# Kernel optimization log

Measured on AMD Instinct MI355X. Metric: run time of the kernel, lower is better.

Reference implementation:

```python
import jax, jax.numpy as jnp
import numpy as np

N = 50000
EPS = 1e-5


def _layernorm(x, g, b):
    mu = jnp.mean(x, axis=-1, keepdims=True)
    var = jnp.mean((x - mu) ** 2, axis=-1, keepdims=True)
    return (x - mu) * jax.lax.rsqrt(var + EPS) * g + b


def _gcn_conv(x, W, b, src, dst, norm, n):
    # PyG GCNConv: x' = D^{-1/2}(A+I)D^{-1/2} (x W) + b, self-loops already in src/dst
    xw = x @ W                                   # [N, F_out]
    msg = xw[src] * norm[:, None]                # gather + scale, [E+N, F_out]
    return jax.ops.segment_sum(msg, dst, num_segments=n) + b


def _prep_edges(edge_index, n):
    loops = jnp.arange(n, dtype=edge_index.dtype)
    src = jnp.concatenate([edge_index[0], loops])
    dst = jnp.concatenate([edge_index[1], loops])
    deg = jax.ops.segment_sum(jnp.ones(dst.shape[0], jnp.float32), dst, num_segments=n)
    dinv = jnp.where(deg > 0, jax.lax.rsqrt(deg), 0.0)
    norm = dinv[src] * dinv[dst]
    return src, dst, norm


def setup_inputs() -> dict:
    key = jax.random.key(0)
    ks = jax.random.split(key, 8)
    gene, hid, nc = 512, 256, 4
    x = jax.random.normal(ks[0], (N, gene), jnp.float32)
    edge_index = jax.random.randint(ks[1], (2, 1600000), 0, N, dtype=jnp.int64)

    def lin(k, fi, fo):
        return jax.random.normal(k, (fi, fo), jnp.float32) / np.sqrt(fi)

    d = {
        "x": x, "edge_index": edge_index,
        "W1": lin(ks[2], gene, hid), "b1": jnp.zeros(hid, jnp.float32),
        "W2": lin(ks[3], hid, 2 * hid), "b2": jnp.zeros(2 * hid, jnp.float32),
        "W3": lin(ks[4], 2 * hid, hid), "b3": jnp.zeros(hid, jnp.float32),
        "W4": lin(ks[5], hid, hid // 2), "b4": jnp.zeros(hid // 2, jnp.float32),
        "Wc": lin(ks[6], hid // 2, nc), "bc": jnp.zeros(nc, jnp.float32),
        "g1": jnp.ones(hid, jnp.float32), "be1": jnp.zeros(hid, jnp.float32),
        "g2": jnp.ones(2 * hid, jnp.float32), "be2": jnp.zeros(2 * hid, jnp.float32),
        "g3": jnp.ones(hid, jnp.float32), "be3": jnp.zeros(hid, jnp.float32),
        "g4": jnp.ones(hid // 2, jnp.float32), "be4": jnp.zeros(hid // 2, jnp.float32),
    }
    return d


def reference(x, edge_index, W1, b1, W2, b2, W3, b3, W4, b4, Wc, bc,
              g1, be1, g2, be2, g3, be3, g4, be4):
    n = x.shape[0]
    src, dst, norm = _prep_edges(edge_index, n)
    # dropout layers are identity (training=False)
    h1 = jax.nn.elu(_layernorm(_gcn_conv(x, W1, b1, src, dst, norm, n), g1, be1))
    h2 = jax.nn.elu(_layernorm(_gcn_conv(h1, W2, b2, src, dst, norm, n), g2, be2))
    h3 = jax.nn.elu(_layernorm(_gcn_conv(h2, W3, b3, src, dst, norm, n), g3, be3))
    h4_in = h3 + h1
    out_conv = _gcn_conv(h4_in, W4, b4, src, dst, norm, n)
    out_bn = _layernorm(out_conv, g4, be4)
    h = jax.nn.elu(out_bn)
    return (h @ Wc + bc, out_conv, out_bn)
```

## Files before the change

### kernel.cpp

```cpp
#include <hip/hip_runtime.h>
#include <hip/hip_bf16.h>
#include <math.h>

typedef unsigned short u16;
typedef u16 us8 __attribute__((ext_vector_type(8)));
typedef u16 us4 __attribute__((ext_vector_type(4)));
typedef float f32x4 __attribute__((ext_vector_type(4)));
typedef float f32x8 __attribute__((ext_vector_type(8)));
typedef __bf16 bf8 __attribute__((ext_vector_type(8)));

#define SCAN_B 256
#define CH 8192

__device__ __forceinline__ float bf2f(u16 v) {
    unsigned u = ((unsigned)v) << 16;
    return __builtin_bit_cast(float, u);
}
__device__ __forceinline__ u16 f2bf(float f) {
    unsigned u = __builtin_bit_cast(unsigned, f);
    unsigned lsb = (u >> 16) & 1;
    u += 0x7fff + lsb;
    return (u16)(u >> 16);
}
__device__ __forceinline__ void fma8(f32x8& acc, float w, us8 v) {
#pragma unroll
    for (int j = 0; j < 8; j++) acc[j] += w * bf2f(v[j]);
}

__global__ void detect_k(const int* __restrict__ ei, int E,
                         const u16* __restrict__ xraw, int* flag) {
    __shared__ int c_i32, c_f32;
    if (threadIdx.x == 0) { c_i32 = 0; c_f32 = 0; }
    __syncthreads();
    int ne = (E < 4096) ? E : 4096;
    for (int e = threadIdx.x; e < ne; e += blockDim.x)
        if (ei[2 * e + 1] != 0) c_i32 = 1;
    for (int k = threadIdx.x; k < 8192; k += blockDim.x) {
        u16 v = xraw[2 * k];
        int ex = (v >> 7) & 0xFF;
        if (ex >= 0xF0) atomicAdd(&c_f32, 1);
    }
    __syncthreads();
    if (threadIdx.x == 0) {
        flag[0] = (c_i32 == 0) ? 1 : 0;
        flag[1] = (c_f32 >= 4) ? 1 : 0;
    }
}

struct WEnt { const void* s; u16* dst; int K; int Nn; int base; };
struct PEnt { const void* s; int n; int off; };
struct PTab { PEnt e[14]; };

#define GX_CVT 4096

__global__ void megacvt_k(const void* __restrict__ xsrc, u16* __restrict__ xdst,
                          long nq, WEnt e0, WEnt e1, WEnt e2, WEnt e3, int wtotal,
                          PTab tab, float* __restrict__ pbuf,
                          const int* __restrict__ flag, int gw) {
    int f32m = flag[1];
    int bid = blockIdx.x;
    if (bid < GX_CVT) {
        long i0 = (long)bid * blockDim.x + threadIdx.x;
        long stride = (long)GX_CVT * blockDim.x;
        if (f32m) {
            const f32x4* s = (const f32x4*)xsrc;
            for (long i = i0; i < nq; i += stride) {
                f32x4 v = s[i];
                us4 o;
                #pragma unroll
                for (int j = 0; j < 4; j++) o[j] = f2bf(v[j]);
                ((us4*)xdst)[i] = o;
            }
        } else {
            const us4* s = (const us4*)xsrc;
            for (long i = i0; i < nq; i += stride) ((us4*)xdst)[i] = s[i];
        }
    } else if (bid < GX_CVT + gw) {
        int t = (bid - GX_CVT) * blockDim.x + threadIdx.x;
        if (t >= wtotal) return;
        WEnt en = (t >= e3.base) ? e3 : ((t >= e2.base) ? e2 : ((t >= e1.base) ? e1 : e0));
        int li = t - en.base;
        int k = li / en.Nn, nn = li - k * en.Nn;
        u16 b;
        if (f32m) b = f2bf(((const float*)en.s)[li]);
        else      b = ((const u16*)en.s)[li];
        en.dst[nn * en.K + k] = b;
    } else {
        PEnt en = tab.e[bid - GX_CVT - gw];
        for (int i = threadIdx.x; i < en.n; i += blockDim.x) {
            float v = f32m ? ((const float*)en.s)[i] : bf2f(((const u16*)en.s)[i]);
            pbuf[en.off + i] = v;
        }
    }
}

__global__ void histA_k(const int* __restrict__ ei, const int* __restrict__ flag,
                        int* __restrict__ hist, int* __restrict__ counts,
                        int E, int n, int NB, int NBUK, int shiftv) {
    __shared__ int lh[256];
    int blk = blockIdx.x;
    int gi = blk * 256 + threadIdx.x;
    if (gi < n) counts[gi] = 1;
    for (int b = threadIdx.x; b < NBUK; b += 256) lh[b] = 0;
    __syncthreads();
    int e0 = blk * CH;
    int e1 = min(e0 + CH, E);
    int i64 = flag[0];
    for (int e = e0 + threadIdx.x; e < e1; e += 256) {
        int d;
        if (i64) d = (int)((const long long*)ei)[(size_t)E + e];
        else     d = ei[(size_t)E + e];
        int b = ((unsigned)d < (unsigned)n) ? min(d >> shiftv, NBUK - 1) : (NBUK - 1);
        atomicAdd(&lh[b], 1);
    }
    __syncthreads();
    for (int b = threadIdx.x; b < NBUK; b += 256) hist[b * NB + blk] = lh[b];
}

__global__ void scan1_k(const int* __restrict__ counts, int* incl, int* bsum, int n) {
    __shared__ int tmp[SCAN_B];
    int t = threadIdx.x;
    int i = blockIdx.x * SCAN_B + t;
    int v = (i < n) ? counts[i] : 0;
    tmp[t] = v;
    __syncthreads();
    for (int o = 1; o < SCAN_B; o <<= 1) {
        int x = 0;
        if (t >= o) x = tmp[t - o];
        __syncthreads();
        if (t >= o) tmp[t] += x;
        __syncthreads();
    }
    if (i < n) incl[i] = tmp[t];
    if (t == SCAN_B - 1) bsum[blockIdx.x] = tmp[t];
}

__global__ void scan2_k(const int* __restrict__ bsum, int* bscan, int nb) {
    __shared__ int tmp[SCAN_B];
    int t = threadIdx.x;
    tmp[t] = (t < nb) ? bsum[t] : 0;
    __syncthreads();
    for (int o = 1; o < SCAN_B; o <<= 1) {
        int x = 0;
        if (t >= o) x = tmp[t - o];
        __syncthreads();
        if (t >= o) tmp[t] += x;
        __syncthreads();
    }
    bscan[t] = tmp[t];
}

__global__ void scatC_k(const int* __restrict__ ei, const int* __restrict__ flag,
                        const int* __restrict__ histincl, const int* __restrict__ bscan,
                        const int* __restrict__ hist, long long* __restrict__ ebuf,
                        int* __restrict__ counts,
                        int E, int n, int NB, int NBUK, int shiftv) {
    __shared__ int cur[256];
    int blk = blockIdx.x;
    for (int b = threadIdx.x; b < NBUK; b += 256) {
        int fi = b * NB + blk;
        int boff = (fi >= 256) ? bscan[(fi >> 8) - 1] : 0;
        cur[b] = histincl[fi] + boff - hist[fi];
    }
    __syncthreads();
    int e0 = blk * CH;
    int e1 = min(e0 + CH, E);
    int i64 = flag[0];
    for (int e = e0 + threadIdx.x; e < e1; e += 256) {
        int s, d;
        if (i64) {
            const long long* e64 = (const long long*)ei;
            s = (int)e64[e]; d = (int)e64[(size_t)E + e];
        } else {
            s = ei[e]; d = ei[(size_t)E + e];
        }
        int b = ((unsigned)d < (unsigned)n) ? min(d >> shiftv, NBUK - 1) : (NBUK - 1);
        int pos = atomicAdd(&cur[b], 1);
        ebuf[pos] = ((long long)(unsigned)d << 32) | (unsigned)s;
        if ((unsigned)d < (unsigned)n) atomicAdd(&counts[d], 1);
    }
}

__global__ void finCSR_k(const int* __restrict__ incl, const int* __restrict__ bscan,
                         const int* __restrict__ counts, int* __restrict__ rowptr,
                         int* __restrict__ cursor, float* __restrict__ dinv, int n) {
    int i = blockIdx.x * SCAN_B + threadIdx.x;
    if (i < n) {
        int boff = (blockIdx.x > 0) ? bscan[blockIdx.x - 1] : 0;
        int rp_end = incl[i] + boff;
        rowptr[i + 1] = rp_end;
        if (i == 0) rowptr[0] = 0;
        cursor[i] = rp_end - counts[i];
        dinv[i] = rsqrtf((float)counts[i]);
    }
}

__global__ void scatD_k(const long long* __restrict__ ebuf, int* cursor,
                        int* __restrict__ col, int E, int n) {
    int e = blockIdx.x * blockDim.x + threadIdx.x;
    if (e < E) {
        long long pr = ebuf[e];
        int d = (int)(pr >> 32);
        int s = (int)(pr & 0xffffffffLL);
        if ((unsigned)s < (unsigned)n && (unsigned)d < (unsigned)n) {
            int pos = atomicAdd(&cursor[d], 1);
            col[pos] = s;
        }
    } else if (e < E + n) {
        int i = e - E;
        int pos = atomicAdd(&cursor[i], 1);
        col[pos] = i;
    }
}

typedef __attribute__((address_space(1))) const void gas_v;
typedef __attribute__((address_space(3))) void las_v;

__global__ __launch_bounds__(256) void gemm128_k(
    const u16* __restrict__ A, const u16* __restrict__ Bt,
    u16* __restrict__ C, int M, int K, int Nn, int nyv) {
    int nx = (M + 127) >> 7;
    int nfull = nx & ~7;
    int cutoff = nfull * nyv;
    int b = blockIdx.x;
    int bx, by;
    if (b < cutoff) {
        int k = b & 7;
        int q = b >> 3;
        by = q % nyv;
        bx = (q / nyv) * 8 + k;
    } else {
        int r = b - cutoff;
        bx = nfull + r / nyv;
        by = r % nyv;
    }

    __shared__ u16 As[128 * 32];
    __shared__ u16 Bs[128 * 32];
    int tid = threadIdx.x;
    int wave = tid >> 6;
    int lane = tid & 63;
    int wr = (wave >> 1) * 64;
    int wc = (wave & 1) * 64;
    long row0 = (long)bx * 128;
    int col0 = by * 128;
    int lr = lane >> 2;
    int lc = lane & 3;
    int m = lane & 15;
    int q = lane >> 4;

    f32x4 acc[4][4];
    #pragma unroll
    for (int i = 0; i < 4; i++)
        #pragma unroll
        for (int j = 0; j < 4; j++) acc[i][j] = (f32x4){0.f, 0.f, 0.f, 0.f};

    for (int k0 = 0; k0 < K; k0 += 32) {
        #pragma unroll
        for (int p = 0; p < 2; p++) {
            int c = wave + p * 4;
            long ar = row0 + c * 16 + lr;
            if (ar > (long)M - 1) ar = (long)M - 1;
            const u16* ga = A + ar * K + k0 + lc * 8;
            __builtin_amdgcn_global_load_lds((gas_v*)ga, (las_v*)&As[c * 512], 16, 0, 0);
            int br = col0 + c * 16 + lr;
            const u16* gb = Bt + (size_t)br * K + k0 + lc * 8;
            __builtin_amdgcn_global_load_lds((gas_v*)gb, (las_v*)&Bs[c * 512], 16, 0, 0);
        }
        __syncthreads();

        us8 av[4], bv[4];
        #pragma unroll
        for (int i = 0; i < 4; i++) {
            av[i] = *(const us8*)&As[(wr + i * 16 + m) * 32 + q * 8];
            bv[i] = *(const us8*)&Bs[(wc + i * 16 + m) * 32 + q * 8];
        }
        #pragma unroll
        for (int i = 0; i < 4; i++) {
            bf8 fa = __builtin_bit_cast(bf8, av[i]);
            #pragma unroll
            for (int j = 0; j < 4; j++) {
                bf8 fb = __builtin_bit_cast(bf8, bv[j]);
                acc[i][j] = __builtin_amdgcn_mfma_f32_16x16x32_bf16(fa, fb, acc[i][j], 0, 0, 0);
            }
        }
        __syncthreads();
    }

    #pragma unroll
    for (int i = 0; i < 4; i++) {
        #pragma unroll
        for (int r = 0; r < 4; r++) {
            long row = row0 + wr + i * 16 + q * 4 + r;
            if (row < M) {
                #pragma unroll
                for (int j = 0; j < 4; j++)
                    C[row * Nn + col0 + wc + j * 16 + m] = f2bf(acc[i][j][r]);
            }
        }
    }
}

template <int F>
__global__ __launch_bounds__(256) void agg_k(
    const u16* __restrict__ in, const int* __restrict__ rowptr,
    const int* __restrict__ col, const float* __restrict__ dinv,
    const float* __restrict__ bias, const float* __restrict__ gamma,
    const float* __restrict__ beta, u16* __restrict__ out_h,
    const u16* __restrict__ resid, void* __restrict__ final_base,
    const int* __restrict__ flag, const float* __restrict__ Wcf,
    const float* __restrict__ bcf, int nN) {
    int wv = threadIdx.x >> 6;
    int lane = threadIdx.x & 63;
    int i = blockIdx.x * 4 + wv;
    if (i >= nN) return;

    constexpr int rowt = F >> 3;
    constexpr int Gw = 64 / rowt;
    int g = lane / rowt;
    int f0 = (lane & (rowt - 1)) << 3;

    int beg = rowptr[i], end = rowptr[i + 1];
    f32x8 acc = {0, 0, 0, 0, 0, 0, 0, 0}, acc2 = acc;
    int e = beg + g;
    for (; e + Gw < end; e += 2 * Gw) {
        int s0 = col[e], s1 = col[e + Gw];
        s0 = ((unsigned)s0 < (unsigned)nN) ? s0 : 0;
        s1 = ((unsigned)s1 < (unsigned)nN) ? s1 : 0;
        float w0 = dinv[s0], w1 = dinv[s1];
        us8 v0 = *(const us8*)(in + (unsigned)(s0 * F) + f0);
        us8 v1 = *(const us8*)(in + (unsigned)(s1 * F) + f0);
        fma8(acc, w0, v0);
        fma8(acc2, w1, v1);
    }
    if (e < end) {
        int s = col[e];
        s = ((unsigned)s < (unsigned)nN) ? s : 0;
        us8 v = *(const us8*)(in + (unsigned)(s * F) + f0);
        fma8(acc, dinv[s], v);
    }
    #pragma unroll
    for (int j = 0; j < 8; j++) acc[j] += acc2[j];

    #pragma unroll
    for (int o = 32; o >= rowt; o >>= 1) {
        #pragma unroll
        for (int j = 0; j < 8; j++) acc[j] += __shfl_down(acc[j], o);
    }
    bool active = lane < rowt;
    float di = dinv[i];

    if (!bias) {
        if (active) {
            us8 o8;
            #pragma unroll
            for (int j = 0; j < 8; j++) o8[j] = f2bf(di * acc[j]);
            *(us8*)(out_h + (unsigned)(i * F) + f0) = o8;
        }
        return;
    }

    f32x8 accv = {0, 0, 0, 0, 0, 0, 0, 0};
    if (active) {
        #pragma unroll
        for (int j = 0; j < 8; j++) accv[j] = di * acc[j] + bias[f0 + j];
    }
    int f32m = final_base ? flag[1] : 0;
    if (final_base && active) {
        size_t conv_idx = (size_t)nN * 4 + (size_t)i * F + f0;
        if (f32m) {
            #pragma unroll
            for (int j = 0; j < 8; j++) ((float*)final_base)[conv_idx + j] = accv[j];
        } else {
            us8 o8;
            #pragma unroll
            for (int j = 0; j < 8; j++) o8[j] = f2bf(accv[j]);
            *(us8*)((u16*)final_base + conv_idx) = o8;
        }
    }

    float p1 = 0.f, p2 = 0.f;
    #pragma unroll
    for (int j = 0; j < 8; j++) { p1 += accv[j]; p2 += accv[j] * accv[j]; }
    #pragma unroll
    for (int o = rowt >> 1; o >= 1; o >>= 1) {
        p1 += __shfl_xor(p1, o);
        p2 += __shfl_xor(p2, o);
    }
    constexpr float invF = 1.0f / (float)F;
    float mu = p1 * invF;
    float var = fmaxf(p2 * invF - mu * mu, 0.f);
    float rstd = rsqrtf(var + 1e-5f);

    f32x8 h8 = {0, 0, 0, 0, 0, 0, 0, 0};
    if (active) {
        f32x8 y8;
        #pragma unroll
        for (int j = 0; j < 8; j++)
            y8[j] = (accv[j] - mu) * rstd * gamma[f0 + j] + beta[f0 + j];
        if (final_base) {
            size_t bn_idx = (size_t)nN * 4 + (size_t)nN * F + (size_t)i * F + f0;
            if (f32m) {
                #pragma unroll
                for (int j = 0; j < 8; j++) ((float*)final_base)[bn_idx + j] = y8[j];
            } else {
                us8 o8;
                #pragma unroll
                for (int j = 0; j < 8; j++) o8[j] = f2bf(y8[j]);
                *(us8*)((u16*)final_base + bn_idx) = o8;
            }
        }
        #pragma unroll
        for (int j = 0; j < 8; j++) h8[j] = (y8[j] > 0.f) ? y8[j] : expm1f(y8[j]);
        if (resid) {
            us8 r8 = *(const us8*)(resid + (unsigned)(i * F) + f0);
            #pragma unroll
            for (int j = 0; j < 8; j++) h8[j] += bf2f(r8[j]);
        }
        if (out_h) {
            us8 o8;
            #pragma unroll
            for (int j = 0; j < 8; j++) o8[j] = f2bf(h8[j]);
            *(us8*)(out_h + (unsigned)(i * F) + f0) = o8;
        }
    }

    if (Wcf) {
        float s0 = 0.f, s1 = 0.f, s2 = 0.f, s3 = 0.f;
        if (active) {
            #pragma unroll
            for (int j = 0; j < 8; j++) {
                const float* wr = Wcf + (f0 + j) * 4;
                s0 += h8[j] * wr[0];
                s1 += h8[j] * wr[1];
                s2 += h8[j] * wr[2];
                s3 += h8[j] * wr[3];
            }
        }
        #pragma unroll
        for (int o = rowt >> 1; o >= 1; o >>= 1) {
            s0 += __shfl_xor(s0, o);
            s1 += __shfl_xor(s1, o);
            s2 += __shfl_xor(s2, o);
            s3 += __shfl_xor(s3, o);
        }
        if (lane == 0) {
            size_t lidx = (size_t)i * 4;
            if (f32m) {
                ((float*)final_base)[lidx + 0] = s0 + bcf[0];
                ((float*)final_base)[lidx + 1] = s1 + bcf[1];
                ((float*)final_base)[lidx + 2] = s2 + bcf[2];
                ((float*)final_base)[lidx + 3] = s3 + bcf[3];
            } else {
                ((u16*)final_base)[lidx + 0] = f2bf(s0 + bcf[0]);
                ((u16*)final_base)[lidx + 1] = f2bf(s1 + bcf[1]);
                ((u16*)final_base)[lidx + 2] = f2bf(s2 + bcf[2]);
                ((u16*)final_base)[lidx + 3] = f2bf(s3 + bcf[3]);
            }
        }
    }
}

__global__ __launch_bounds__(256) void ln_elu_k(u16* __restrict__ h,
                                                const float* __restrict__ bias,
                                                const float* __restrict__ gamma,
                                                const float* __restrict__ beta, int nN) {
    int wv = threadIdx.x >> 6;
    int lane = threadIdx.x & 63;
    int i = blockIdx.x * 4 + wv;
    if (i >= nN) return;
    int f0 = lane * 8;
    size_t base = (size_t)i * 512 + f0;
    us8 v8 = *(const us8*)(h + base);
    f32x8 v;
    #pragma unroll
    for (int j = 0; j < 8; j++) v[j] = bf2f(v8[j]) + bias[f0 + j];
    float p1 = 0.f, p2 = 0.f;
    #pragma unroll
    for (int j = 0; j < 8; j++) { p1 += v[j]; p2 += v[j] * v[j]; }
    #pragma unroll
    for (int o = 32; o >= 1; o >>= 1) {
        p1 += __shfl_xor(p1, o);
        p2 += __shfl_xor(p2, o);
    }
    const float invF = 1.0f / 512.0f;
    float mu = p1 * invF;
    float var = fmaxf(p2 * invF - mu * mu, 0.f);
    float rstd = rsqrtf(var + 1e-5f);
    us8 o8;
    #pragma unroll
    for (int j = 0; j < 8; j++) {
        float y = (v[j] - mu) * rstd * gamma[f0 + j] + beta[f0 + j];
        y = (y > 0.f) ? y : expm1f(y);
        o8[j] = f2bf(y);
    }
    *(us8*)(h + base) = o8;
}

__global__ void marker_k(float* out) {
    if (threadIdx.x == 0 && blockIdx.x == 0) {
        out[0] = 31337.0f; out[1] = 31337.0f;
    }
}

extern "C" void kernel_launch(void* const* d_in, const int* in_sizes, int n_in,
                              void* d_out, int out_size, void* d_ws, size_t ws_size,
                              hipStream_t stream) {
    const int N = in_sizes[0] / 512;
    const int E = in_sizes[1] / 2;

    const void* x  = d_in[0];
    const int* ei  = (const int*)d_in[1];

    char* p = (char*)d_ws;
    auto alloc = [&](size_t bytes) -> void* {
        void* r = (void*)p;
        p += (bytes + 255) & ~(size_t)255;
        return r;
    };
    int*   flag   = (int*)alloc(256);
    int*   counts = (int*)alloc((size_t)N * 4);
    int*   rowptr = (int*)alloc((size_t)(N + 1) * 4);
    int*   cursor = (int*)alloc((size_t)N * 4);
    int*   incl   = (int*)alloc((size_t)N * 4);
    int*   bsum   = (int*)alloc(256 * 4);
    int*   bscan  = (int*)alloc(256 * 4);
    float* dinv   = (float*)alloc((size_t)N * 4);
    int*   col    = (int*)alloc((size_t)(E + N) * 4);
    float* pbuf   = (float*)alloc(4096 * 4);
    u16* W1t = (u16*)alloc((size_t)512 * 256 * 2);
    u16* W2t = (u16*)alloc((size_t)256 * 512 * 2);
    u16* W3t = (u16*)alloc((size_t)512 * 256 * 2);
    u16* W4t = (u16*)alloc((size_t)256 * 128 * 2);
    u16* bigA = (u16*)alloc((size_t)N * 512 * 2);
    u16* xw   = (u16*)alloc((size_t)N * 256 * 2);
    u16* h1   = (u16*)alloc((size_t)N * 256 * 2);

    size_t needed = (size_t)(p - (char*)d_ws);
    if (needed > ws_size) {
        marker_k<<<1, 64, 0, stream>>>((float*)d_out);
        return;
    }

    u16* xbf = bigA;
    u16* h2  = bigA;

    int shiftv = 8;
    while (((N - 1) >> shiftv) > 255) shiftv++;
    int NBUK = ((N - 1) >> shiftv) + 1;
    int NB_E = (E + CH - 1) / CH;
    int flatlen = NBUK * NB_E;
    int NH = (flatlen + 255) / 256;
    long long* ebuf = (long long*)xw;
    int* hist     = (int*)h1;
    int* histincl = hist + flatlen;
    int* ofs      = histincl + flatlen;

    PTab tab;
    tab.e[0]  = { d_in[3],  256, 0    };
    tab.e[1]  = { d_in[12], 256, 256  };
    tab.e[2]  = { d_in[13], 256, 512  };
    tab.e[3]  = { d_in[5],  512, 768  };
    tab.e[4]  = { d_in[14], 512, 1280 };
    tab.e[5]  = { d_in[15], 512, 1792 };
    tab.e[6]  = { d_in[7],  256, 2304 };
    tab.e[7]  = { d_in[16], 256, 2560 };
    tab.e[8]  = { d_in[17], 256, 2816 };
    tab.e[9]  = { d_in[9],  128, 3072 };
    tab.e[10] = { d_in[18], 128, 3200 };
    tab.e[11] = { d_in[19], 128, 3328 };
    tab.e[12] = { d_in[10], 512, 3456 };
    tab.e[13] = { d_in[11], 4,   3968 };
    float* b1f = pbuf + 0,   *g1f = pbuf + 256,  *be1f = pbuf + 512;
    float* b2f = pbuf + 768, *g2f = pbuf + 1280, *be2f = pbuf + 1792;
    float* b3f = pbuf + 2304,*g3f = pbuf + 2560, *be3f = pbuf + 2816;
    float* b4f = pbuf + 3072,*g4f = pbuf + 3200, *be4f = pbuf + 3328;
    float* Wcf = pbuf + 3456,*bcf = pbuf + 3968;

    int NB = (N + SCAN_B - 1) / SCAN_B;

    detect_k<<<1, 256, 0, stream>>>(ei, E, (const u16*)x, flag);

    {
        WEnt e0 = { d_in[2], W1t, 512, 256, 0 };
        WEnt e1 = { d_in[4], W2t, 256, 512, 512 * 256 };
        WEnt e2 = { d_in[6], W3t, 512, 256, 512 * 256 + 256 * 512 };
        WEnt e3 = { d_in[8], W4t, 256, 128, 512 * 256 * 2 + 256 * 512 };
        int wtotal = 512 * 256 * 2 + 256 * 512 + 256 * 128;
        int gw = (wtotal + 255) / 256;
        megacvt_k<<<GX_CVT + gw + 14, 256, 0, stream>>>(
            x, xbf, (long)N * 512 / 4, e0, e1, e2, e3, wtotal, tab, pbuf, flag, gw);
    }

    histA_k<<<NB_E, 256, 0, stream>>>(ei, flag, hist, counts, E, N, NB_E, NBUK, shiftv);
    scan1_k<<<NH, SCAN_B, 0, stream>>>(hist, histincl, bsum, flatlen);
    scan2_k<<<1, SCAN_B, 0, stream>>>(bsum, bscan, NH);
    scatC_k<<<NB_E, 256, 0, stream>>>(ei, flag, histincl, bscan, hist, ebuf, counts,
                                      E, N, NB_E, NBUK, shiftv);
    scan1_k<<<NB, SCAN_B, 0, stream>>>(counts, incl, bsum, N);
    scan2_k<<<1, SCAN_B, 0, stream>>>(bsum, bscan, NB);
    finCSR_k<<<NB, SCAN_B, 0, stream>>>(incl, bscan, counts, rowptr, cursor, dinv, N);
    scatD_k<<<(E + N + 255) / 256, 256, 0, stream>>>(ebuf, cursor, col, E, N);

    int gx = (N + 127) / 128;
    int ga = (N + 3) / 4;

    gemm128_k<<<gx * 2, 256, 0, stream>>>(xbf, W1t, xw, N, 512, 256, 2);
    agg_k<256><<<ga, 256, 0, stream>>>(xw, rowptr, col, dinv, b1f, g1f, be1f,
                                       h1, nullptr, nullptr, flag, nullptr, nullptr, N);
    agg_k<256><<<ga, 256, 0, stream>>>(h1, rowptr, col, dinv, nullptr, nullptr, nullptr,
                                       xw, nullptr, nullptr, flag, nullptr, nullptr, N);
    gemm128_k<<<gx * 4, 256, 0, stream>>>(xw, W2t, h2, N, 256, 512, 4);
    ln_elu_k<<<ga, 256, 0, stream>>>(h2, b2f, g2f, be2f, N);
    gemm128_k<<<gx * 2, 256, 0, stream>>>(h2, W3t, xw, N, 512, 256, 2);
    agg_k<256><<<ga, 256, 0, stream>>>(xw, rowptr, col, dinv, b3f, g3f, be3f,
                                       h1, h1, nullptr, flag, nullptr, nullptr, N);
    gemm128_k<<<gx * 1, 256, 0, stream>>>(h1, W4t, xw, N, 256, 128, 1);
    agg_k<128><<<ga, 256, 0, stream>>>(xw, rowptr, col, dinv, b4f, g4f, be4f,
                                       nullptr, nullptr, d_out, flag, Wcf, bcf, N);
}
```

Baseline: 970.6 us.

## Double-buffer LDS tiles in bf16 MFMA GEMM to overlap loads with compute

Changes the GEMM mainloop to use two LDS buffers per operand. The next K-slice is issued via global_load_lds before the MFMAs on the current slice, and the per-iteration address math is hoisted out of the loop. This aims to hide global-load latency behind matrix math and removes one barrier per iteration. In exchange it doubles LDS use per block, which may reduce occupancy. It also drops an unused pointer.

After: 965.7 us. No clear change (-0.5%).

```diff
diff --git a/kernel.cpp b/kernel.cpp
--- a/kernel.cpp
+++ b/kernel.cpp
@@ -235,8 +235,8 @@
         by = r % nyv;
     }
 
-    __shared__ u16 As[128 * 32];
-    __shared__ u16 Bs[128 * 32];
+    __shared__ u16 As[2][128 * 32];
+    __shared__ u16 Bs[2][128 * 32];
     int tid = threadIdx.x;
     int wave = tid >> 6;
     int lane = tid & 63;
@@ -249,31 +249,45 @@
     int m = lane & 15;
     int q = lane >> 4;
 
+    long ar0 = row0 + (wave + 0) * 16 + lr;
+    long ar1 = row0 + (wave + 4) * 16 + lr;
+    if (ar0 > (long)M - 1) ar0 = (long)M - 1;
+    if (ar1 > (long)M - 1) ar1 = (long)M - 1;
+    const u16* gA0 = A + ar0 * K + lc * 8;
+    const u16* gA1 = A + ar1 * K + lc * 8;
+    const u16* gB0 = Bt + (size_t)(col0 + (wave + 0) * 16 + lr) * K + lc * 8;
+    const u16* gB1 = Bt + (size_t)(col0 + (wave + 4) * 16 + lr) * K + lc * 8;
+    int lds0 = (wave + 0) * 512;
+    int lds1 = (wave + 4) * 512;
+
     f32x4 acc[4][4];
     #pragma unroll
     for (int i = 0; i < 4; i++)
         #pragma unroll
         for (int j = 0; j < 4; j++) acc[i][j] = (f32x4){0.f, 0.f, 0.f, 0.f};
 
+    __builtin_amdgcn_global_load_lds((gas_v*)(gA0), (las_v*)&As[0][lds0], 16, 0, 0);
+    __builtin_amdgcn_global_load_lds((gas_v*)(gA1), (las_v*)&As[0][lds1], 16, 0, 0);
+    __builtin_amdgcn_global_load_lds((gas_v*)(gB0), (las_v*)&Bs[0][lds0], 16, 0, 0);
+    __builtin_amdgcn_global_load_lds((gas_v*)(gB1), (las_v*)&Bs[0][lds1], 16, 0, 0);
+    __syncthreads();
+
+    int cur = 0;
     for (int k0 = 0; k0 < K; k0 += 32) {
-        #pragma unroll
-        for (int p = 0; p < 2; p++) {
-            int c = wave + p * 4;
-            long ar = row0 + c * 16 + lr;
-            if (ar > (long)M - 1) ar = (long)M - 1;
-            const u16* ga = A + ar * K + k0 + lc * 8;
-            __builtin_amdgcn_global_load_lds((gas_v*)ga, (las_v*)&As[c * 512], 16, 0, 0);
-            int br = col0 + c * 16 + lr;
-            const u16* gb = Bt + (size_t)br * K + k0 + lc * 8;
-            __builtin_amdgcn_global_load_lds((gas_v*)gb, (las_v*)&Bs[c * 512], 16, 0, 0);
-        }
-        __syncthreads();
+        if (k0 + 32 < K) {
+            int nb = cur ^ 1;
+            int ko = k0 + 32;
+            __builtin_amdgcn_global_load_lds((gas_v*)(gA0 + ko), (las_v*)&As[nb][lds0], 16, 0, 0);
+            __builtin_amdgcn_global_load_lds((gas_v*)(gA1 + ko), (las_v*)&As[nb][lds1], 16, 0, 0);
+            __builtin_amdgcn_global_load_lds((gas_v*)(gB0 + ko), (las_v*)&Bs[nb][lds0], 16, 0, 0);
+            __builtin_amdgcn_global_load_lds((gas_v*)(gB1 + ko), (las_v*)&Bs[nb][lds1], 16, 0, 0);
+        }
 
         us8 av[4], bv[4];
         #pragma unroll
         for (int i = 0; i < 4; i++) {
-            av[i] = *(const us8*)&As[(wr + i * 16 + m) * 32 + q * 8];
-            bv[i] = *(const us8*)&Bs[(wc + i * 16 + m) * 32 + q * 8];
+            av[i] = *(const us8*)&As[cur][(wr + i * 16 + m) * 32 + q * 8];
+            bv[i] = *(const us8*)&Bs[cur][(wc + i * 16 + m) * 32 + q * 8];
         }
         #pragma unroll
         for (int i = 0; i < 4; i++) {
@@ -285,6 +299,7 @@
             }
         }
         __syncthreads();
+        cur ^= 1;
     }
 
     #pragma unroll
@@ -554,7 +569,6 @@
     long long* ebuf = (long long*)xw;
     int* hist     = (int*)h1;
     int* histincl = hist + flatlen;
-    int* ofs      = histincl + flatlen;
 
     PTab tab;
     tab.e[0]  = { d_in[3],  256, 0    };
```
